# Kernel tuning notes

Hardware: AMD Instinct MI355X
Metric: run time of the kernel (lower is better)

## Reference

```python
import jax, jax.numpy as jnp
import numpy as np

B, S, D, H = 8, 2048, 1024, 4
HD = D // H


def _layernorm(x, w, b, eps=1e-5):
    mu = jnp.mean(x, axis=-1, keepdims=True)
    var = jnp.mean((x - mu) ** 2, axis=-1, keepdims=True)
    return (x - mu) * jax.lax.rsqrt(var + eps) * w + b


def setup_inputs() -> dict:
    key = jax.random.key(0)
    ks = jax.random.split(key, 10)
    s = 1.0 / np.sqrt(D)
    return {
        "text_representation": jax.random.normal(ks[0], (B, S, D), jnp.float32),
        "image_representation": jax.random.normal(ks[1], (B, S, D), jnp.float32),
        "ln_t_w": jnp.ones((D,), jnp.float32),
        "ln_t_b": jnp.zeros((D,), jnp.float32),
        "ln_i_w": jnp.ones((D,), jnp.float32),
        "ln_i_b": jnp.zeros((D,), jnp.float32),
        "Wa": jax.random.uniform(ks[2], (H, HD, D), jnp.float32, -s, s),
        "Wa_b": jax.random.uniform(ks[3], (H, HD), jnp.float32, -s, s),
        "Wq": jax.random.uniform(ks[4], (H, HD, D), jnp.float32, -s, s),
        "Wq_b": jax.random.uniform(ks[5], (H, HD), jnp.float32, -s, s),
        "sim_w": jax.random.uniform(ks[6], (HD, 1), jnp.float32, -1.0, 1.0),
        "sim_b": jax.random.uniform(ks[7], (HD,), jnp.float32, -1.0, 1.0),
        "fc_w": jax.random.uniform(ks[8], (1, H * HD), jnp.float32, -s, s),
        "fc_b": jax.random.uniform(ks[9], (1,), jnp.float32, -s, s),
    }


def reference(text_representation, image_representation, ln_t_w, ln_t_b,
              ln_i_w, ln_i_b, Wa, Wa_b, Wq, Wq_b, sim_w, sim_b, fc_w, fc_b):
    eps_cos = 1e-6
    text_rep = _layernorm(text_representation, ln_t_w, ln_t_b)   # [B,S,D]
    image_rep = _layernorm(image_representation, ln_i_w, ln_i_b)  # [B,S,D]
    # cosine similarity along last dim (torch-style norm clamping)
    tn = jnp.maximum(jnp.linalg.norm(text_rep, axis=-1), eps_cos)
    im = jnp.maximum(jnp.linalg.norm(image_rep, axis=-1), eps_cos)
    per_pos_sim = jnp.sum(text_rep * image_rep, axis=-1) / (tn * im)  # [B,S]
    global_sim = jnp.mean(per_pos_sim, axis=1, keepdims=True)          # [B,1]
    text_global = jnp.mean(text_rep, axis=1)    # [B,D]
    image_global = jnp.mean(image_rep, axis=1)  # [B,D]
    gate_a = jnp.einsum('bd,hkd->bhk', text_global, Wa) + Wa_b    # [B,H,HD]
    gate_q = jnp.einsum('bd,hkd->bhk', image_global, Wq) + Wq_b   # [B,H,HD]
    sim_feat = global_sim * sim_w[:, 0] + sim_b                   # [B,HD]
    gates = jax.nn.relu(gate_a + gate_q + sim_feat[:, None, :])   # [B,H,HD]
    combined = gates.reshape(gates.shape[0], H * HD)              # [B,H*HD]
    final_gate = jax.nn.sigmoid(combined @ fc_w.T + fc_b)         # [B,1]
    g = final_gate[:, :, None]                                    # [B,1,1]
    return g * text_rep + (1.0 - g) * image_rep
```

## Files before the change

### kernel.cpp

```cpp
#include <hip/hip_runtime.h>
#include <math.h>

#define BB 8
#define SS 2048
#define DD 1024
#define HH 4
#define HDD 256
#define NROW (BB*SS)
#define RW 4

#define OFF_MU_T 0
#define OFF_RS_T (NROW)
#define OFF_MU_I (2*NROW)
#define OFF_RS_I (3*NROW)
#define OFF_TG   (4*NROW)
#define OFF_IG   (4*NROW + BB*DD)
#define OFF_SIM  (4*NROW + 2*BB*DD)
#define OFF_LOGIT (OFF_SIM + BB)
#define ZERO_CNT (2*BB*DD + 2*BB)

__device__ __forceinline__ float wred(float v) {
#pragma unroll
  for (int m = 32; m > 0; m >>= 1) v += __shfl_xor(v, m, 64);
  return v;
}

__global__ __launch_bounds__(256) void kz(float* p, int n) {
  int i = blockIdx.x * 256 + threadIdx.x;
  if (i < n) p[i] = 0.f;
}

__global__ __launch_bounds__(256) void k1_stats(
    const float* __restrict__ text, const float* __restrict__ image,
    const float* __restrict__ wt, const float* __restrict__ bt,
    const float* __restrict__ wi, const float* __restrict__ bi,
    float* __restrict__ ws)
{
  const int tid  = threadIdx.x;
  const int lane = tid & 63;
  const int wv   = tid >> 6;
  const int wave_id = blockIdx.x * 4 + wv;
  const int row0 = wave_id * RW;
  const int b    = row0 >> 11;
  const int c0   = lane << 2;

  float4 wt4[4], bt4[4], wi4[4], bi4[4];
#pragma unroll
  for (int c = 0; c < 4; ++c) {
    wt4[c] = *(const float4*)(wt + c*256 + c0);
    bt4[c] = *(const float4*)(bt + c*256 + c0);
    wi4[c] = *(const float4*)(wi + c*256 + c0);
    bi4[c] = *(const float4*)(bi + c*256 + c0);
  }

  float tga[16], iga[16];
#pragma unroll
  for (int j = 0; j < 16; ++j) { tga[j] = 0.f; iga[j] = 0.f; }
  float sim_loc = 0.f;

  for (int r = 0; r < RW; ++r) {
    const int row = row0 + r;
    const float* tp = text  + (size_t)row * DD;
    const float* ip = image + (size_t)row * DD;
    float4 t4[4], i4[4];
#pragma unroll
    for (int c = 0; c < 4; ++c) {
      t4[c] = *(const float4*)(tp + c*256 + c0);
      i4[c] = *(const float4*)(ip + c*256 + c0);
    }
    float st=0.f, sst=0.f, si=0.f, ssi=0.f;
#pragma unroll
    for (int c = 0; c < 4; ++c) {
      st  += t4[c].x + t4[c].y + t4[c].z + t4[c].w;
      sst += t4[c].x*t4[c].x + t4[c].y*t4[c].y + t4[c].z*t4[c].z + t4[c].w*t4[c].w;
      si  += i4[c].x + i4[c].y + i4[c].z + i4[c].w;
      ssi += i4[c].x*i4[c].x + i4[c].y*i4[c].y + i4[c].z*i4[c].z + i4[c].w*i4[c].w;
    }
    st = wred(st); sst = wred(sst); si = wred(si); ssi = wred(ssi);
    const float invD = 1.f/DD;
    const float mt = st*invD,  vt = sst*invD - mt*mt;
    const float mi = si*invD,  vi = ssi*invD - mi*mi;
    const float rt = rsqrtf(vt + 1e-5f);
    const float ri = rsqrtf(vi + 1e-5f);
    if (lane == 0) {
      ws[OFF_MU_T+row]=mt; ws[OFF_RS_T+row]=rt;
      ws[OFF_MU_I+row]=mi; ws[OFF_RS_I+row]=ri;
    }
    float dv=0.f, nt2=0.f, ni2=0.f;
#pragma unroll
    for (int c = 0; c < 4; ++c) {
      const float tv[4] = {t4[c].x, t4[c].y, t4[c].z, t4[c].w};
      const float iv[4] = {i4[c].x, i4[c].y, i4[c].z, i4[c].w};
      const float wtv[4] = {wt4[c].x, wt4[c].y, wt4[c].z, wt4[c].w};
      const float btv[4] = {bt4[c].x, bt4[c].y, bt4[c].z, bt4[c].w};
      const float wiv[4] = {wi4[c].x, wi4[c].y, wi4[c].z, wi4[c].w};
      const float biv[4] = {bi4[c].x, bi4[c].y, bi4[c].z, bi4[c].w};
#pragma unroll
      for (int j = 0; j < 4; ++j) {
        const float tn  = (tv[j]-mt)*rt*wtv[j] + btv[j];
        const float inn = (iv[j]-mi)*ri*wiv[j] + biv[j];
        tga[c*4+j] += tn;  iga[c*4+j] += inn;
        dv += tn*inn;  nt2 += tn*tn;  ni2 += inn*inn;
      }
    }
    dv = wred(dv); nt2 = wred(nt2); ni2 = wred(ni2);
    const float nt = fmaxf(sqrtf(nt2), 1e-6f);
    const float ni = fmaxf(sqrtf(ni2), 1e-6f);
    sim_loc += dv / (nt*ni);
  }

  __shared__ float accs[2][4][DD];
  __shared__ float sim_s[4];
#pragma unroll
  for (int c = 0; c < 4; ++c) {
    *(float4*)&accs[0][wv][c*256 + c0] = make_float4(tga[c*4+0], tga[c*4+1], tga[c*4+2], tga[c*4+3]);
    *(float4*)&accs[1][wv][c*256 + c0] = make_float4(iga[c*4+0], iga[c*4+1], iga[c*4+2], iga[c*4+3]);
  }
  if (lane == 0) sim_s[wv] = sim_loc;
  __syncthreads();
  const int col0 = tid << 2;
#pragma unroll
  for (int j = 0; j < 4; ++j) {
    const float ts = accs[0][0][col0+j] + accs[0][1][col0+j] + accs[0][2][col0+j] + accs[0][3][col0+j];
    const float is = accs[1][0][col0+j] + accs[1][1][col0+j] + accs[1][2][col0+j] + accs[1][3][col0+j];
    atomicAdd(&ws[OFF_TG + b*DD + col0 + j], ts);
    atomicAdd(&ws[OFF_IG + b*DD + col0 + j], is);
  }
  if (tid == 0) atomicAdd(&ws[OFF_SIM + b], sim_s[0]+sim_s[1]+sim_s[2]+sim_s[3]);
}

__global__ __launch_bounds__(256) void k2_gates(
    const float* __restrict__ Wa, const float* __restrict__ Wab,
    const float* __restrict__ Wq, const float* __restrict__ Wqb,
    const float* __restrict__ simw, const float* __restrict__ simb,
    const float* __restrict__ fcw, float* __restrict__ ws)
{
  const int tid  = threadIdx.x;
  const int lane = tid & 63;
  const int wv   = tid >> 6;
  const int r0   = blockIdx.x * 4;
  const int d0   = tid << 2;

  __shared__ float red[4][4][BB];

  for (int rr = 0; rr < 4; ++rr) {
    const int r = r0 + rr;
    const float4 a4 = *(const float4*)(Wa + (size_t)r*DD + d0);
    const float4 q4 = *(const float4*)(Wq + (size_t)r*DD + d0);
    float acc[BB];
#pragma unroll
    for (int b = 0; b < BB; ++b) {
      const float4 t = *(const float4*)(ws + OFF_TG + b*DD + d0);
      const float4 i = *(const float4*)(ws + OFF_IG + b*DD + d0);
      acc[b] = a4.x*t.x + a4.y*t.y + a4.z*t.z + a4.w*t.w
             + q4.x*i.x + q4.y*i.y + q4.z*i.z + q4.w*i.w;
    }
#pragma unroll
    for (int b = 0; b < BB; ++b) {
      acc[b] = wred(acc[b]);
      if (lane == 0) red[rr][wv][b] = acc[b];
    }
  }
  __syncthreads();
  if (tid < BB) {
    const int b = tid;
    const float inv = 1.f/SS;
    const float gs = ws[OFF_SIM + b] * inv;
    float part = 0.f;
#pragma unroll
    for (int rr = 0; rr < 4; ++rr) {
      const int r = r0 + rr;
      const int k = r & 255;
      const float v = (red[rr][0][b] + red[rr][1][b] + red[rr][2][b] + red[rr][3][b]) * inv;
      float gate = v + Wab[r] + Wqb[r] + gs*simw[k] + simb[k];
      gate = fmaxf(gate, 0.f);
      part += gate * fcw[r];
    }
    atomicAdd(&ws[OFF_LOGIT + b], part);
  }
}

__global__ __launch_bounds__(256) void k3_blend(
    const float* __restrict__ text, const float* __restrict__ image,
    const float* __restrict__ wt, const float* __restrict__ bt,
    const float* __restrict__ wi, const float* __restrict__ bi,
    const float* __restrict__ fcb,
    const float* __restrict__ ws, float* __restrict__ out)
{
  const int row = blockIdx.x;
  const int b   = row >> 11;
  const int d0  = threadIdx.x << 2;
  const float g  = 1.f / (1.f + expf(-(ws[OFF_LOGIT+b] + fcb[0])));
  const float gi = 1.f - g;
  const float mt = ws[OFF_MU_T+row], rt = ws[OFF_RS_T+row];
  const float mi = ws[OFF_MU_I+row], ri = ws[OFF_RS_I+row];
  const float4 t4  = *(const float4*)(text  + (size_t)row*DD + d0);
  const float4 i4  = *(const float4*)(image + (size_t)row*DD + d0);
  const float4 wt4 = *(const float4*)(wt + d0);
  const float4 bt4 = *(const float4*)(bt + d0);
  const float4 wi4 = *(const float4*)(wi + d0);
  const float4 bi4 = *(const float4*)(bi + d0);
  float4 o;
  o.x = g*((t4.x-mt)*rt*wt4.x + bt4.x) + gi*((i4.x-mi)*ri*wi4.x + bi4.x);
  o.y = g*((t4.y-mt)*rt*wt4.y + bt4.y) + gi*((i4.y-mi)*ri*wi4.y + bi4.y);
  o.z = g*((t4.z-mt)*rt*wt4.z + bt4.z) + gi*((i4.z-mi)*ri*wi4.z + bi4.z);
  o.w = g*((t4.w-mt)*rt*wt4.w + bt4.w) + gi*((i4.w-mi)*ri*wi4.w + bi4.w);
  *(float4*)(out + (size_t)row*DD + d0) = o;
}

extern "C" void kernel_launch(void* const* d_in, const int* in_sizes, int n_in,
                              void* d_out, int out_size, void* d_ws, size_t ws_size,
                              hipStream_t stream)
{
  const float* text   = (const float*)d_in[0];
  const float* image  = (const float*)d_in[1];
  const float* ln_t_w = (const float*)d_in[2];
  const float* ln_t_b = (const float*)d_in[3];
  const float* ln_i_w = (const float*)d_in[4];
  const float* ln_i_b = (const float*)d_in[5];
  const float* Wa     = (const float*)d_in[6];
  const float* Wab    = (const float*)d_in[7];
  const float* Wq     = (const float*)d_in[8];
  const float* Wqb    = (const float*)d_in[9];
  const float* simw   = (const float*)d_in[10];
  const float* simb   = (const float*)d_in[11];
  const float* fcw    = (const float*)d_in[12];
  const float* fcb    = (const float*)d_in[13];
  float* ws  = (float*)d_ws;
  float* out = (float*)d_out;

  kz<<<(ZERO_CNT + 255) / 256, 256, 0, stream>>>(ws + OFF_TG, ZERO_CNT);
  k1_stats<<<NROW / (4*RW), 256, 0, stream>>>(text, image, ln_t_w, ln_t_b, ln_i_w, ln_i_b, ws);
  k2_gates<<<HH*HDD/4, 256, 0, stream>>>(Wa, Wab, Wq, Wqb, simw, simb, fcw, ws);
  k3_blend<<<NROW, 256, 0, stream>>>(text, image, ln_t_w, ln_t_b, ln_i_w, ln_i_b, fcb, ws, out);
}
```

Before: 292.3 us.

## Replace atomic global-mean accumulation with per-slice partials and a separate reduce kernel

The stats kernel changes from one wave per four rows to one block per row, with 8 rows per block and a software prefetch of the next row. It writes per-slice partial sums to the workspace instead of issuing atomicAdds, and a new reduce kernel sums those partials deterministically, which also removes the zeroing kernel. The blend kernel now handles two rows per block with the gate folded into the scale factors. The cost is two __syncthreads per row in the stats kernel and an extra 2x2048x1024 float partial buffer that is written and then read back.

```diff
diff --git a/kernel.cpp b/kernel.cpp
--- a/kernel.cpp
+++ b/kernel.cpp
@@ -7,27 +7,25 @@
 #define HH 4
 #define HDD 256
 #define NROW (BB*SS)
-#define RW 4
+#define G 8
+#define NSLICE (NROW/G)
 
 #define OFF_MU_T 0
-#define OFF_RS_T (NROW)
+#define OFF_RS_T NROW
 #define OFF_MU_I (2*NROW)
 #define OFF_RS_I (3*NROW)
-#define OFF_TG   (4*NROW)
-#define OFF_IG   (4*NROW + BB*DD)
-#define OFF_SIM  (4*NROW + 2*BB*DD)
+#define OFF_PT   (4*NROW)
+#define OFF_PI   (OFF_PT + NSLICE*DD)
+#define OFF_PS   (OFF_PI + NSLICE*DD)
+#define OFF_TG   (OFF_PS + NSLICE)
+#define OFF_IG   (OFF_TG + BB*DD)
+#define OFF_SIM  (OFF_IG + BB*DD)
 #define OFF_LOGIT (OFF_SIM + BB)
-#define ZERO_CNT (2*BB*DD + 2*BB)
 
 __device__ __forceinline__ float wred(float v) {
 #pragma unroll
   for (int m = 32; m > 0; m >>= 1) v += __shfl_xor(v, m, 64);
   return v;
-}
-
-__global__ __launch_bounds__(256) void kz(float* p, int n) {
-  int i = blockIdx.x * 256 + threadIdx.x;
-  if (i < n) p[i] = 0.f;
 }
 
 __global__ __launch_bounds__(256) void k1_stats(
@@ -36,97 +34,114 @@
     const float* __restrict__ wi, const float* __restrict__ bi,
     float* __restrict__ ws)
 {
+  const int g    = blockIdx.x;
   const int tid  = threadIdx.x;
   const int lane = tid & 63;
   const int wv   = tid >> 6;
-  const int wave_id = blockIdx.x * 4 + wv;
-  const int row0 = wave_id * RW;
-  const int b    = row0 >> 11;
-  const int c0   = lane << 2;
-
-  float4 wt4[4], bt4[4], wi4[4], bi4[4];
-#pragma unroll
-  for (int c = 0; c < 4; ++c) {
-    wt4[c] = *(const float4*)(wt + c*256 + c0);
-    bt4[c] = *(const float4*)(bt + c*256 + c0);
-    wi4[c] = *(const float4*)(wi + c*256 + c0);
-    bi4[c] = *(const float4*)(bi + c*256 + c0);
-  }
-
-  float tga[16], iga[16];
-#pragma unroll
-  for (int j = 0; j < 16; ++j) { tga[j] = 0.f; iga[j] = 0.f; }
+  const int d0   = tid << 2;
+  const int row0 = g * G;
+
+  __shared__ float red1[4][4];
+  __shared__ float red2[4][4];
+
+  const float4 wt4 = *(const float4*)(wt + d0);
+  const float4 bt4 = *(const float4*)(bt + d0);
+  const float4 wi4 = *(const float4*)(wi + d0);
+  const float4 bi4 = *(const float4*)(bi + d0);
+
+  float4 tga = make_float4(0.f,0.f,0.f,0.f);
+  float4 iga = make_float4(0.f,0.f,0.f,0.f);
   float sim_loc = 0.f;
 
-  for (int r = 0; r < RW; ++r) {
-    const int row = row0 + r;
-    const float* tp = text  + (size_t)row * DD;
-    const float* ip = image + (size_t)row * DD;
-    float4 t4[4], i4[4];
-#pragma unroll
-    for (int c = 0; c < 4; ++c) {
-      t4[c] = *(const float4*)(tp + c*256 + c0);
-      i4[c] = *(const float4*)(ip + c*256 + c0);
-    }
-    float st=0.f, sst=0.f, si=0.f, ssi=0.f;
-#pragma unroll
-    for (int c = 0; c < 4; ++c) {
-      st  += t4[c].x + t4[c].y + t4[c].z + t4[c].w;
-      sst += t4[c].x*t4[c].x + t4[c].y*t4[c].y + t4[c].z*t4[c].z + t4[c].w*t4[c].w;
-      si  += i4[c].x + i4[c].y + i4[c].z + i4[c].w;
-      ssi += i4[c].x*i4[c].x + i4[c].y*i4[c].y + i4[c].z*i4[c].z + i4[c].w*i4[c].w;
-    }
-    st = wred(st); sst = wred(sst); si = wred(si); ssi = wred(ssi);
+  float4 ct = *(const float4*)(text  + (size_t)row0*DD + d0);
+  float4 ci = *(const float4*)(image + (size_t)row0*DD + d0);
+
+  for (int r = 0; r < G; ++r) {
+    float4 nt_ = ct, ni_ = ci;
+    if (r + 1 < G) {
+      nt_ = *(const float4*)(text  + (size_t)(row0+r+1)*DD + d0);
+      ni_ = *(const float4*)(image + (size_t)(row0+r+1)*DD + d0);
+    }
+    float s1 = ct.x + ct.y + ct.z + ct.w;
+    float s2 = ct.x*ct.x + ct.y*ct.y + ct.z*ct.z + ct.w*ct.w;
+    float s3 = ci.x + ci.y + ci.z + ci.w;
+    float s4 = ci.x*ci.x + ci.y*ci.y + ci.z*ci.z + ci.w*ci.w;
+    s1 = wred(s1); s2 = wred(s2); s3 = wred(s3); s4 = wred(s4);
+    if (lane == 0) { red1[wv][0]=s1; red1[wv][1]=s2; red1[wv][2]=s3; red1[wv][3]=s4; }
+    __syncthreads();
+    const float st  = red1[0][0]+red1[1][0]+red1[2][0]+red1[3][0];
+    const float sst = red1[0][1]+red1[1][1]+red1[2][1]+red1[3][1];
+    const float si  = red1[0][2]+red1[1][2]+red1[2][2]+red1[3][2];
+    const float ssi = red1[0][3]+red1[1][3]+red1[2][3]+red1[3][3];
     const float invD = 1.f/DD;
     const float mt = st*invD,  vt = sst*invD - mt*mt;
     const float mi = si*invD,  vi = ssi*invD - mi*mi;
     const float rt = rsqrtf(vt + 1e-5f);
     const float ri = rsqrtf(vi + 1e-5f);
-    if (lane == 0) {
+    if (tid == 0) {
+      const int row = row0 + r;
       ws[OFF_MU_T+row]=mt; ws[OFF_RS_T+row]=rt;
       ws[OFF_MU_I+row]=mi; ws[OFF_RS_I+row]=ri;
     }
-    float dv=0.f, nt2=0.f, ni2=0.f;
-#pragma unroll
-    for (int c = 0; c < 4; ++c) {
-      const float tv[4] = {t4[c].x, t4[c].y, t4[c].z, t4[c].w};
-      const float iv[4] = {i4[c].x, i4[c].y, i4[c].z, i4[c].w};
-      const float wtv[4] = {wt4[c].x, wt4[c].y, wt4[c].z, wt4[c].w};
-      const float btv[4] = {bt4[c].x, bt4[c].y, bt4[c].z, bt4[c].w};
-      const float wiv[4] = {wi4[c].x, wi4[c].y, wi4[c].z, wi4[c].w};
-      const float biv[4] = {bi4[c].x, bi4[c].y, bi4[c].z, bi4[c].w};
-#pragma unroll
-      for (int j = 0; j < 4; ++j) {
-        const float tn  = (tv[j]-mt)*rt*wtv[j] + btv[j];
-        const float inn = (iv[j]-mi)*ri*wiv[j] + biv[j];
-        tga[c*4+j] += tn;  iga[c*4+j] += inn;
-        dv += tn*inn;  nt2 += tn*tn;  ni2 += inn*inn;
-      }
-    }
+    float4 tn, in_;
+    tn.x  = (ct.x-mt)*rt*wt4.x + bt4.x;  tn.y  = (ct.y-mt)*rt*wt4.y + bt4.y;
+    tn.z  = (ct.z-mt)*rt*wt4.z + bt4.z;  tn.w  = (ct.w-mt)*rt*wt4.w + bt4.w;
+    in_.x = (ci.x-mi)*ri*wi4.x + bi4.x;  in_.y = (ci.y-mi)*ri*wi4.y + bi4.y;
+    in_.z = (ci.z-mi)*ri*wi4.z + bi4.z;  in_.w = (ci.w-mi)*ri*wi4.w + bi4.w;
+    tga.x += tn.x; tga.y += tn.y; tga.z += tn.z; tga.w += tn.w;
+    iga.x += in_.x; iga.y += in_.y; iga.z += in_.z; iga.w += in_.w;
+    float dv  = tn.x*in_.x + tn.y*in_.y + tn.z*in_.z + tn.w*in_.w;
+    float nt2 = tn.x*tn.x + tn.y*tn.y + tn.z*tn.z + tn.w*tn.w;
+    float ni2 = in_.x*in_.x + in_.y*in_.y + in_.z*in_.z + in_.w*in_.w;
     dv = wred(dv); nt2 = wred(nt2); ni2 = wred(ni2);
-    const float nt = fmaxf(sqrtf(nt2), 1e-6f);
-    const float ni = fmaxf(sqrtf(ni2), 1e-6f);
-    sim_loc += dv / (nt*ni);
-  }
-
-  __shared__ float accs[2][4][DD];
-  __shared__ float sim_s[4];
-#pragma unroll
-  for (int c = 0; c < 4; ++c) {
-    *(float4*)&accs[0][wv][c*256 + c0] = make_float4(tga[c*4+0], tga[c*4+1], tga[c*4+2], tga[c*4+3]);
-    *(float4*)&accs[1][wv][c*256 + c0] = make_float4(iga[c*4+0], iga[c*4+1], iga[c*4+2], iga[c*4+3]);
-  }
-  if (lane == 0) sim_s[wv] = sim_loc;
-  __syncthreads();
-  const int col0 = tid << 2;
-#pragma unroll
-  for (int j = 0; j < 4; ++j) {
-    const float ts = accs[0][0][col0+j] + accs[0][1][col0+j] + accs[0][2][col0+j] + accs[0][3][col0+j];
-    const float is = accs[1][0][col0+j] + accs[1][1][col0+j] + accs[1][2][col0+j] + accs[1][3][col0+j];
-    atomicAdd(&ws[OFF_TG + b*DD + col0 + j], ts);
-    atomicAdd(&ws[OFF_IG + b*DD + col0 + j], is);
-  }
-  if (tid == 0) atomicAdd(&ws[OFF_SIM + b], sim_s[0]+sim_s[1]+sim_s[2]+sim_s[3]);
+    if (lane == 0) { red2[wv][0]=dv; red2[wv][1]=nt2; red2[wv][2]=ni2; }
+    __syncthreads();
+    if (tid == 0) {
+      const float d_all = red2[0][0]+red2[1][0]+red2[2][0]+red2[3][0];
+      const float nt = fmaxf(sqrtf(red2[0][1]+red2[1][1]+red2[2][1]+red2[3][1]), 1e-6f);
+      const float ni = fmaxf(sqrtf(red2[0][2]+red2[1][2]+red2[2][2]+red2[3][2]), 1e-6f);
+      sim_loc += d_all / (nt*ni);
+    }
+    ct = nt_; ci = ni_;
+  }
+  *(float4*)(ws + OFF_PT + (size_t)g*DD + d0) = tga;
+  *(float4*)(ws + OFF_PI + (size_t)g*DD + d0) = iga;
+  if (tid == 0) ws[OFF_PS + g] = sim_loc;
+}
+
+__global__ __launch_bounds__(256) void kR_reduce(float* __restrict__ ws)
+{
+  const int tid = threadIdx.x;
+  if (blockIdx.x < 32) {
+    const int b  = blockIdx.x >> 2;
+    const int ch = blockIdx.x & 3;
+    const int d  = ch*256 + tid;
+    const float* pt = ws + OFF_PT + (size_t)(b*256)*DD + d;
+    const float* pi = ws + OFF_PI + (size_t)(b*256)*DD + d;
+    float at = 0.f, ai = 0.f;
+#pragma unroll 4
+    for (int s = 0; s < 256; ++s) {
+      at += pt[(size_t)s*DD];
+      ai += pi[(size_t)s*DD];
+    }
+    ws[OFF_TG + b*DD + d] = at;
+    ws[OFF_IG + b*DD + d] = ai;
+  } else {
+    __shared__ float sred[256];
+    const int b = tid >> 5, j = tid & 31;
+    float a = 0.f;
+#pragma unroll
+    for (int k = 0; k < 8; ++k) a += ws[OFF_PS + b*256 + j*8 + k];
+    sred[tid] = a;
+    __syncthreads();
+    if (j == 0) {
+      float s = 0.f;
+#pragma unroll
+      for (int m = 0; m < 32; ++m) s += sred[b*32 + m];
+      ws[OFF_SIM + b] = s;
+    }
+    if (tid < BB) ws[OFF_LOGIT + tid] = 0.f;
+  }
 }
 
 __global__ __launch_bounds__(256) void k2_gates(
@@ -187,25 +202,42 @@
     const float* __restrict__ fcb,
     const float* __restrict__ ws, float* __restrict__ out)
 {
-  const int row = blockIdx.x;
-  const int b   = row >> 11;
-  const int d0  = threadIdx.x << 2;
-  const float g  = 1.f / (1.f + expf(-(ws[OFF_LOGIT+b] + fcb[0])));
-  const float gi = 1.f - g;
-  const float mt = ws[OFF_MU_T+row], rt = ws[OFF_RS_T+row];
-  const float mi = ws[OFF_MU_I+row], ri = ws[OFF_RS_I+row];
-  const float4 t4  = *(const float4*)(text  + (size_t)row*DD + d0);
-  const float4 i4  = *(const float4*)(image + (size_t)row*DD + d0);
+  const int r0 = blockIdx.x * 2;
+  const int b  = r0 >> 11;
+  const int d0 = threadIdx.x << 2;
+
+  const float4 ta = *(const float4*)(text  + (size_t)r0*DD + d0);
+  const float4 ia = *(const float4*)(image + (size_t)r0*DD + d0);
+  const float4 tb = *(const float4*)(text  + (size_t)(r0+1)*DD + d0);
+  const float4 ib = *(const float4*)(image + (size_t)(r0+1)*DD + d0);
   const float4 wt4 = *(const float4*)(wt + d0);
   const float4 bt4 = *(const float4*)(bt + d0);
   const float4 wi4 = *(const float4*)(wi + d0);
   const float4 bi4 = *(const float4*)(bi + d0);
-  float4 o;
-  o.x = g*((t4.x-mt)*rt*wt4.x + bt4.x) + gi*((i4.x-mi)*ri*wi4.x + bi4.x);
-  o.y = g*((t4.y-mt)*rt*wt4.y + bt4.y) + gi*((i4.y-mi)*ri*wi4.y + bi4.y);
-  o.z = g*((t4.z-mt)*rt*wt4.z + bt4.z) + gi*((i4.z-mi)*ri*wi4.z + bi4.z);
-  o.w = g*((t4.w-mt)*rt*wt4.w + bt4.w) + gi*((i4.w-mi)*ri*wi4.w + bi4.w);
-  *(float4*)(out + (size_t)row*DD + d0) = o;
+
+  const float g  = 1.f / (1.f + expf(-(ws[OFF_LOGIT+b] + fcb[0])));
+  const float gi = 1.f - g;
+
+  const float mta = ws[OFF_MU_T+r0],   rta = ws[OFF_RS_T+r0];
+  const float mia = ws[OFF_MU_I+r0],   ria = ws[OFF_RS_I+r0];
+  const float mtb = ws[OFF_MU_T+r0+1], rtb = ws[OFF_RS_T+r0+1];
+  const float mib = ws[OFF_MU_I+r0+1], rib = ws[OFF_RS_I+r0+1];
+
+  const float gta = g*rta, gia = gi*ria;
+  const float gtb = g*rtb, gib = gi*rib;
+
+  float4 oa, ob;
+  oa.x = gta*(ta.x-mta)*wt4.x + g*bt4.x + gia*(ia.x-mia)*wi4.x + gi*bi4.x;
+  oa.y = gta*(ta.y-mta)*wt4.y + g*bt4.y + gia*(ia.y-mia)*wi4.y + gi*bi4.y;
+  oa.z = gta*(ta.z-mta)*wt4.z + g*bt4.z + gia*(ia.z-mia)*wi4.z + gi*bi4.z;
+  oa.w = gta*(ta.w-mta)*wt4.w + g*bt4.w + gia*(ia.w-mia)*wi4.w + gi*bi4.w;
+  ob.x = gtb*(tb.x-mtb)*wt4.x + g*bt4.x + gib*(ib.x-mib)*wi4.x + gi*bi4.x;
+  ob.y = gtb*(tb.y-mtb)*wt4.y + g*bt4.y + gib*(ib.y-mib)*wi4.y + gi*bi4.y;
+  ob.z = gtb*(tb.z-mtb)*wt4.z + g*bt4.z + gib*(ib.z-mib)*wi4.z + gi*bi4.z;
+  ob.w = gtb*(tb.w-mtb)*wt4.w + g*bt4.w + gib*(ib.w-mib)*wi4.w + gi*bi4.w;
+
+  *(float4*)(out + (size_t)r0*DD + d0)     = oa;
+  *(float4*)(out + (size_t)(r0+1)*DD + d0) = ob;
 }
 
 extern "C" void kernel_launch(void* const* d_in, const int* in_sizes, int n_in,
@@ -229,8 +261,8 @@
   float* ws  = (float*)d_ws;
   float* out = (float*)d_out;
 
-  kz<<<(ZERO_CNT + 255) / 256, 256, 0, stream>>>(ws + OFF_TG, ZERO_CNT);
-  k1_stats<<<NROW / (4*RW), 256, 0, stream>>>(text, image, ln_t_w, ln_t_b, ln_i_w, ln_i_b, ws);
+  k1_stats<<<NSLICE, 256, 0, stream>>>(text, image, ln_t_w, ln_t_b, ln_i_w, ln_i_b, ws);
+  kR_reduce<<<33, 256, 0, stream>>>(ws);
   k2_gates<<<HH*HDD/4, 256, 0, stream>>>(Wa, Wab, Wq, Wqb, simw, simb, fcw, ws);
-  k3_blend<<<NROW, 256, 0, stream>>>(text, image, ln_t_w, ln_t_b, ln_i_w, ln_i_b, fcb, ws, out);
-}
+  k3_blend<<<NROW/2, 256, 0, stream>>>(text, image, ln_t_w, ln_t_b, ln_i_w, ln_i_b, fcb, ws, out);
+}
```

Result: faster. 272.2 us (-6.9%).
